# Kernel optimization log

Measured on AMD Instinct MI355X. Metric: run time of the kernel, lower is better.

## Reference

```python
import jax, jax.numpy as jnp
import numpy as np

N, E, IN_DIM, OUT_DIM, T = 100000, 1600000, 128, 64, 8
V_THRESHOLD = 1.0
EPS = 1e-7

# ---- Lorentz manifold (curvature -1), time coordinate first ----

def _linner(a, b):
    # Lorentzian inner product <a,b>_L = -a0*b0 + sum_i ai*bi
    return -a[..., 0] * b[..., 0] + jnp.sum(a[..., 1:] * b[..., 1:], axis=-1)

def _proju(z, u):
    # project ambient vector u to tangent space at z (<z,z>_L = -1)
    return u + _linner(z, u)[..., None] * z

def _expmap(z, u):
    un = jnp.sqrt(jnp.maximum(_linner(u, u), EPS))[..., None]
    return jnp.cosh(un) * z + jnp.sinh(un) * u / un

def _dist0(z):
    # geodesic distance to origin o=(1,0,...,0): arccosh(-<o,z>_L) = arccosh(z0)
    return jnp.arccosh(jnp.maximum(z[..., 0], 1.0 + EPS))

# ---- GCNConv (torch_geometric semantics: self-loops + symmetric norm) ----

def _gcn(x, edge_index, W, b):
    src, dst = edge_index[0], edge_index[1]
    loops = jnp.arange(N, dtype=src.dtype)
    src = jnp.concatenate([src, loops])
    dst = jnp.concatenate([dst, loops])
    deg = jax.ops.segment_sum(jnp.ones_like(dst, dtype=x.dtype), dst, num_segments=N)
    dinv = jax.lax.rsqrt(jnp.maximum(deg, 1.0))  # deg >= 1 due to self-loops
    norm = dinv[src] * dinv[dst]                 # [E+N]
    h = x @ W                                    # [N, OUT_DIM]
    out = jax.ops.segment_sum(norm[:, None] * h[src], dst, num_segments=N)
    return out + b


def setup_inputs() -> dict:
    key = jax.random.key(0)
    k1, k2, k3 = jax.random.split(key, 3)
    x = jax.random.normal(k1, (N, IN_DIM), dtype=jnp.float32)
    edge_index = jax.random.randint(k2, (2, E), 0, N, dtype=jnp.int32)
    W = jax.random.normal(k3, (IN_DIM, OUT_DIM), dtype=jnp.float32) / np.sqrt(IN_DIM)
    b = jnp.zeros((OUT_DIM,), dtype=jnp.float32)
    return {"x": x, "edge_index": edge_index, "W": W, "b": b}


def reference(x, edge_index, W, b):
    h = _gcn(x, edge_index, W, b)                       # [N, D]
    origin = jnp.zeros_like(h).at[..., 0].set(1.0)      # manifold origin
    x_seq = jnp.broadcast_to(h, (T,) + h.shape)         # [T, N, D]

    def step(z, x_t):
        u = _proju(z, x_t)                              # input current in T_z M
        z_new = _expmap(z, u)                           # charge along geodesic
        v = _dist0(z_new)                               # membrane potential [N]
        spike = v >= V_THRESHOLD
        z_out = jnp.where(spike[..., None], origin, z_new)  # hard reset
        return z_out, (spike.astype(h.dtype), z_out)

    _, (o_seq, z_seq) = jax.lax.scan(step, origin, x_seq)
    return o_seq, z_seq  # [T, N], [T, N, D]
```

## Files before the change

### kernel.cpp

```cpp
#include <hip/hip_runtime.h>
#include <math.h>

#define IN_DIM_C 128
#define OUT_DIM_C 64
#define T_STEPS 8
#define KC_MAX 512
#define PTILE 2048
#define GKC 32

__device__ __forceinline__ float4 f4zero() { return make_float4(0.f, 0.f, 0.f, 0.f); }

__global__ __launch_bounds__(64) void k_scanK(const int* __restrict__ chist,
                                              int* __restrict__ gcursor,
                                              int* __restrict__ offsets,
                                              int kc, int n, int E) {
    int lane = threadIdx.x;
    int carry = 0;
    for (int c = 0; c * 64 < kc; ++c) {
        int idx = c * 64 + lane;
        int v = (idx < kc) ? chist[idx] : 0;
        int x = v;
        #pragma unroll
        for (int off = 1; off < 64; off <<= 1) {
            int t = __shfl_up(x, off, 64);
            if (lane >= off) x += t;
        }
        if (idx < kc) gcursor[idx] = carry + x - v;
        carry += __shfl(x, 63, 64);
    }
    if (lane == 0) offsets[n] = E;
}

__global__ __launch_bounds__(256) void k_gemm_hist(const float* __restrict__ x,
                                                   const float* __restrict__ W,
                                                   float* __restrict__ h,
                                                   const int* __restrict__ dst,
                                                   int* __restrict__ chist,
                                                   int n, int E, int gemm_blocks) {
    __shared__ __align__(16) float smem[GKC * 132 + GKC * OUT_DIM_C];

    if ((int)blockIdx.x < gemm_blocks) {
        float* xs = smem;
        float* Ws = smem + GKC * 132;
        const int tid = threadIdx.x;
        const int cg = tid & 7;
        const int ng = tid >> 3;
        const int node_base = blockIdx.x * 128;

        float acc[4][8];
        #pragma unroll
        for (int i = 0; i < 4; ++i)
            #pragma unroll
            for (int j = 0; j < 8; ++j) acc[i][j] = 0.f;

        #pragma unroll 1
        for (int c = 0; c < IN_DIM_C / GKC; ++c) {
            __syncthreads();
            #pragma unroll
            for (int i = 0; i < 4; ++i) {
                int idx = tid + i * 256;
                int nd = idx >> 3, k4 = idx & 7;
                int node = node_base + nd;
                float4 v = f4zero();
                if (node < n) v = *(const float4*)&x[(long)node * IN_DIM_C + c * GKC + k4 * 4];
                xs[(k4 * 4 + 0) * 132 + nd] = v.x;
                xs[(k4 * 4 + 1) * 132 + nd] = v.y;
                xs[(k4 * 4 + 2) * 132 + nd] = v.z;
                xs[(k4 * 4 + 3) * 132 + nd] = v.w;
            }
            #pragma unroll
            for (int i = 0; i < 2; ++i) {
                int idx = tid + i * 256;
                ((float4*)Ws)[idx] = ((const float4*)&W[c * GKC * OUT_DIM_C])[idx];
            }
            __syncthreads();

            #pragma unroll
            for (int k = 0; k < GKC; ++k) {
                float4 a = *(const float4*)&xs[k * 132 + ng * 4];
                const float* wr = &Ws[k * OUT_DIM_C + cg * 8];
                float4 b0 = *(const float4*)&wr[0];
                float4 b1 = *(const float4*)&wr[4];
                #pragma unroll
                for (int i = 0; i < 4; ++i) {
                    float av = (i == 0) ? a.x : (i == 1) ? a.y : (i == 2) ? a.z : a.w;
                    acc[i][0] = fmaf(av, b0.x, acc[i][0]);
                    acc[i][1] = fmaf(av, b0.y, acc[i][1]);
                    acc[i][2] = fmaf(av, b0.z, acc[i][2]);
                    acc[i][3] = fmaf(av, b0.w, acc[i][3]);
                    acc[i][4] = fmaf(av, b1.x, acc[i][4]);
                    acc[i][5] = fmaf(av, b1.y, acc[i][5]);
                    acc[i][6] = fmaf(av, b1.z, acc[i][6]);
                    acc[i][7] = fmaf(av, b1.w, acc[i][7]);
                }
            }
        }

        #pragma unroll
        for (int i = 0; i < 4; ++i) {
            int node = node_base + ng * 4 + i;
            if (node < n) {
                *(float4*)&h[(long)node * OUT_DIM_C + cg * 8] =
                    make_float4(acc[i][0], acc[i][1], acc[i][2], acc[i][3]);
                *(float4*)&h[(long)node * OUT_DIM_C + cg * 8 + 4] =
                    make_float4(acc[i][4], acc[i][5], acc[i][6], acc[i][7]);
            }
        }
    } else {
        int* hh = (int*)smem;
        const int tid = threadIdx.x;
        int hb = blockIdx.x - gemm_blocks;
        for (int i = tid; i < KC_MAX; i += 256) hh[i] = 0;
        __syncthreads();
        long base = (long)hb * 4096;
        #pragma unroll
        for (int j = 0; j < 16; ++j) {
            long e = base + j * 256 + tid;
            if (e < E) atomicAdd(&hh[dst[e] >> 8], 1);
        }
        __syncthreads();
        for (int i = tid; i < KC_MAX; i += 256)
            if (hh[i]) atomicAdd(&chist[i], hh[i]);
    }
}

__global__ __launch_bounds__(256) void k_part(const int* __restrict__ src,
                                              const int* __restrict__ dst,
                                              int* __restrict__ gcursor,
                                              int* __restrict__ part, int E, int kc) {
    __shared__ int hist[KC_MAX];
    __shared__ int offs[KC_MAX];
    __shared__ int cur[KC_MAX];
    __shared__ int gbase[KC_MAX];
    const int tid = threadIdx.x;
    long base = (long)blockIdx.x * PTILE;

    for (int i = tid; i < KC_MAX; i += 256) hist[i] = 0;
    __syncthreads();
    #pragma unroll
    for (int j = 0; j < PTILE / 256; ++j) {
        long e = base + j * 256 + tid;
        if (e < E) atomicAdd(&hist[dst[e] >> 8], 1);
    }
    __syncthreads();
    if (tid < 64) {
        int carry = 0;
        for (int c = 0; c * 64 < kc; ++c) {
            int idx = c * 64 + tid;
            int v = (idx < kc) ? hist[idx] : 0;
            int x = v;
            #pragma unroll
            for (int off = 1; off < 64; off <<= 1) {
                int t = __shfl_up(x, off, 64);
                if (tid >= off) x += t;
            }
            if (idx < kc) { offs[idx] = carry + x - v; cur[idx] = carry + x - v; }
            carry += __shfl(x, 63, 64);
        }
    }
    __syncthreads();
    for (int b = tid; b < kc; b += 256)
        gbase[b] = hist[b] ? atomicAdd(&gcursor[b], hist[b]) : 0;
    __syncthreads();
    #pragma unroll
    for (int j = 0; j < PTILE / 256; ++j) {
        long e = base + j * 256 + tid;
        if (e < E) {
            int d = dst[e];
            int b = d >> 8;
            int r = atomicAdd(&cur[b], 1);
            part[gbase[b] + r - offs[b]] = (src[e] << 8) | (d & 255);
        }
    }
}

__global__ __launch_bounds__(256) void k_sort(const int* __restrict__ part,
                                              const int* __restrict__ gcursor,
                                              int* __restrict__ part2,
                                              int* __restrict__ offsets,
                                              float* __restrict__ dinv, int n) {
    __shared__ int cnt[256];
    __shared__ int cur[256];
    __shared__ int wsum[4], woff[4];
    const int tid = threadIdx.x;
    const int bkt = blockIdx.x;
    int start = bkt ? gcursor[bkt - 1] : 0;
    int end = gcursor[bkt];

    cnt[tid] = 0;
    __syncthreads();
    for (int i = start + tid; i < end; i += 256)
        atomicAdd(&cnt[part[i] & 255], 1);
    __syncthreads();

    int v = cnt[tid];
    int lane = tid & 63, wv = tid >> 6;
    int x = v;
    #pragma unroll
    for (int off = 1; off < 64; off <<= 1) {
        int t = __shfl_up(x, off, 64);
        if (lane >= off) x += t;
    }
    if (lane == 63) wsum[wv] = x;
    __syncthreads();
    if (tid == 0) { int c = 0; for (int w = 0; w < 4; ++w) { woff[w] = c; c += wsum[w]; } }
    __syncthreads();
    int myloc = woff[wv] + x - v;
    cur[tid] = myloc;
    int node = (bkt << 8) + tid;
    if (node < n) {
        offsets[node] = start + myloc;
        dinv[node] = rsqrtf((float)(v + 1));
    }
    __syncthreads();

    for (int i = start + tid; i < end; i += 256) {
        int p = part[i];
        int r = atomicAdd(&cur[p & 255], 1);
        part2[start + r] = ((unsigned)p) >> 8;
    }
}

__global__ __launch_bounds__(256) void k_pullspike(const int* __restrict__ offsets,
                                                   const int* __restrict__ part2,
                                                   const float* __restrict__ dinv,
                                                   const float* __restrict__ h,
                                                   const float* __restrict__ b,
                                                   float* __restrict__ o_seq,
                                                   float* __restrict__ z_seq, int n) {
    int gid = blockIdx.x * 256 + threadIdx.x;
    int node = gid >> 4;
    int sub = threadIdx.x & 15;
    if (node >= n) return;
    const float s0 = (sub == 0) ? -1.0f : 1.0f;
    int lane0 = (threadIdx.x & 63) & ~15;

    int o0 = offsets[node], o1 = offsets[node + 1];
    float dd = dinv[node];
    float4 hv = *(const float4*)&h[(long)node * OUT_DIM_C + sub * 4];
    float4 bv = *(const float4*)&b[sub * 4];
    float dd2 = dd * dd;
    float4 g = make_float4(fmaf(dd2, hv.x, bv.x), fmaf(dd2, hv.y, bv.y),
                           fmaf(dd2, hv.z, bv.z), fmaf(dd2, hv.w, bv.w));
    int i = o0;
    for (; i + 8 <= o1; i += 8) {
        int sa0 = part2[i],     sa1 = part2[i + 1], sa2 = part2[i + 2], sa3 = part2[i + 3];
        int sa4 = part2[i + 4], sa5 = part2[i + 5], sa6 = part2[i + 6], sa7 = part2[i + 7];
        float w0 = dinv[sa0] * dd, w1 = dinv[sa1] * dd, w2 = dinv[sa2] * dd, w3 = dinv[sa3] * dd;
        float w4 = dinv[sa4] * dd, w5 = dinv[sa5] * dd, w6 = dinv[sa6] * dd, w7 = dinv[sa7] * dd;
        float4 h0 = *(const float4*)&h[(long)sa0 * OUT_DIM_C + sub * 4];
        float4 h1 = *(const float4*)&h[(long)sa1 * OUT_DIM_C + sub * 4];
        float4 h2 = *(const float4*)&h[(long)sa2 * OUT_DIM_C + sub * 4];
        float4 h3 = *(const float4*)&h[(long)sa3 * OUT_DIM_C + sub * 4];
        float4 h4 = *(const float4*)&h[(long)sa4 * OUT_DIM_C + sub * 4];
        float4 h5 = *(const float4*)&h[(long)sa5 * OUT_DIM_C + sub * 4];
        float4 h6 = *(const float4*)&h[(long)sa6 * OUT_DIM_C + sub * 4];
        float4 h7 = *(const float4*)&h[(long)sa7 * OUT_DIM_C + sub * 4];
        g.x = fmaf(w0, h0.x, g.x); g.y = fmaf(w0, h0.y, g.y);
        g.z = fmaf(w0, h0.z, g.z); g.w = fmaf(w0, h0.w, g.w);
        g.x = fmaf(w1, h1.x, g.x); g.y = fmaf(w1, h1.y, g.y);
        g.z = fmaf(w1, h1.z, g.z); g.w = fmaf(w1, h1.w, g.w);
        g.x = fmaf(w2, h2.x, g.x); g.y = fmaf(w2, h2.y, g.y);
        g.z = fmaf(w2, h2.z, g.z); g.w = fmaf(w2, h2.w, g.w);
        g.x = fmaf(w3, h3.x, g.x); g.y = fmaf(w3, h3.y, g.y);
        g.z = fmaf(w3, h3.z, g.z); g.w = fmaf(w3, h3.w, g.w);
        g.x = fmaf(w4, h4.x, g.x); g.y = fmaf(w4, h4.y, g.y);
        g.z = fmaf(w4, h4.z, g.z); g.w = fmaf(w4, h4.w, g.w);
        g.x = fmaf(w5, h5.x, g.x); g.y = fmaf(w5, h5.y, g.y);
        g.z = fmaf(w5, h5.z, g.z); g.w = fmaf(w5, h5.w, g.w);
        g.x = fmaf(w6, h6.x, g.x); g.y = fmaf(w6, h6.y, g.y);
        g.z = fmaf(w6, h6.z, g.z); g.w = fmaf(w6, h6.w, g.w);
        g.x = fmaf(w7, h7.x, g.x); g.y = fmaf(w7, h7.y, g.y);
        g.z = fmaf(w7, h7.z, g.z); g.w = fmaf(w7, h7.w, g.w);
    }
    for (; i + 4 <= o1; i += 4) {
        int sa0 = part2[i], sa1 = part2[i + 1], sa2 = part2[i + 2], sa3 = part2[i + 3];
        float w0 = dinv[sa0] * dd, w1 = dinv[sa1] * dd;
        float w2 = dinv[sa2] * dd, w3 = dinv[sa3] * dd;
        float4 h0 = *(const float4*)&h[(long)sa0 * OUT_DIM_C + sub * 4];
        float4 h1 = *(const float4*)&h[(long)sa1 * OUT_DIM_C + sub * 4];
        float4 h2 = *(const float4*)&h[(long)sa2 * OUT_DIM_C + sub * 4];
        float4 h3 = *(const float4*)&h[(long)sa3 * OUT_DIM_C + sub * 4];
        g.x = fmaf(w0, h0.x, g.x); g.y = fmaf(w0, h0.y, g.y);
        g.z = fmaf(w0, h0.z, g.z); g.w = fmaf(w0, h0.w, g.w);
        g.x = fmaf(w1, h1.x, g.x); g.y = fmaf(w1, h1.y, g.y);
        g.z = fmaf(w1, h1.z, g.z); g.w = fmaf(w1, h1.w, g.w);
        g.x = fmaf(w2, h2.x, g.x); g.y = fmaf(w2, h2.y, g.y);
        g.z = fmaf(w2, h2.z, g.z); g.w = fmaf(w2, h2.w, g.w);
        g.x = fmaf(w3, h3.x, g.x); g.y = fmaf(w3, h3.y, g.y);
        g.z = fmaf(w3, h3.z, g.z); g.w = fmaf(w3, h3.w, g.w);
    }
    for (; i < o1; ++i) {
        int s = part2[i];
        float w = dinv[s] * dd;
        float4 h0 = *(const float4*)&h[(long)s * OUT_DIM_C + sub * 4];
        g.x = fmaf(w, h0.x, g.x); g.y = fmaf(w, h0.y, g.y);
        g.z = fmaf(w, h0.z, g.z); g.w = fmaf(w, h0.w, g.w);
    }

    float4 origin = f4zero();
    if (sub == 0) origin.x = 1.0f;

    auto step = [&](float4 z, float4& zn, bool& sp) {
        float p = s0 * z.x * g.x + z.y * g.y + z.z * g.z + z.w * g.w;
        p += __shfl_xor(p, 1, 64);
        p += __shfl_xor(p, 2, 64);
        p += __shfl_xor(p, 4, 64);
        p += __shfl_xor(p, 8, 64);
        float4 u = make_float4(fmaf(p, z.x, g.x), fmaf(p, z.y, g.y),
                               fmaf(p, z.z, g.z), fmaf(p, z.w, g.w));
        float q = s0 * u.x * u.x + u.y * u.y + u.z * u.z + u.w * u.w;
        q += __shfl_xor(q, 1, 64);
        q += __shfl_xor(q, 2, 64);
        q += __shfl_xor(q, 4, 64);
        q += __shfl_xor(q, 8, 64);
        float un = sqrtf(fmaxf(q, 1e-7f));
        float c = coshf(un);
        float sh = sinhf(un) / un;
        zn = make_float4(fmaf(c, z.x, sh * u.x), fmaf(c, z.y, sh * u.y),
                         fmaf(c, z.z, sh * u.z), fmaf(c, z.w, sh * u.w));
        float z0 = __shfl(zn.x, lane0, 64);
        float v = acoshf(fmaxf(z0, 1.0f + 1e-7f));
        sp = (v >= 1.0f);
    };

    float4 z1; bool sp0;
    step(origin, z1, sp0);
    float4 r0 = sp0 ? origin : z1;

    float4 z = origin;
    bool at0 = true;
    for (int t = 0; t < T_STEPS; ++t) {
        float4 zn; bool sp;
        if (at0) { sp = sp0; zn = r0; }
        else {
            step(z, zn, sp);
            if (sp) zn = origin;
        }
        *(float4*)&z_seq[(long)t * n * OUT_DIM_C + (long)node * OUT_DIM_C + sub * 4] = zn;
        if (sub == 0) o_seq[(long)t * n + node] = sp ? 1.0f : 0.0f;
        z = zn;
        at0 = sp;
    }
}

__global__ __launch_bounds__(256) void k_hist(const int* __restrict__ dst,
                                              int* __restrict__ chist, int E) {
    __shared__ int hh[KC_MAX];
    const int tid = threadIdx.x;
    for (int i = tid; i < KC_MAX; i += 256) hh[i] = 0;
    __syncthreads();
    long base = (long)blockIdx.x * 4096;
    #pragma unroll
    for (int j = 0; j < 16; ++j) {
        long e = base + j * 256 + tid;
        if (e < E) atomicAdd(&hh[dst[e] >> 8], 1);
    }
    __syncthreads();
    for (int i = tid; i < KC_MAX; i += 256)
        if (hh[i]) atomicAdd(&chist[i], hh[i]);
}

__global__ __launch_bounds__(256) void k_gemm(const float* __restrict__ x,
                                              const float* __restrict__ W,
                                              float* __restrict__ h, int n) {
    __shared__ __align__(16) float xs[GKC * 132];
    __shared__ __align__(16) float Ws[GKC * OUT_DIM_C];

    const int tid = threadIdx.x;
    const int cg = tid & 7;
    const int ng = tid >> 3;
    const int node_base = blockIdx.x * 128;

    float acc[4][8];
    #pragma unroll
    for (int i = 0; i < 4; ++i)
        #pragma unroll
        for (int j = 0; j < 8; ++j) acc[i][j] = 0.f;

    #pragma unroll 1
    for (int c = 0; c < IN_DIM_C / GKC; ++c) {
        __syncthreads();
        #pragma unroll
        for (int i = 0; i < 4; ++i) {
            int idx = tid + i * 256;
            int nd = idx >> 3, k4 = idx & 7;
            int node = node_base + nd;
            float4 v = f4zero();
            if (node < n) v = *(const float4*)&x[(long)node * IN_DIM_C + c * GKC + k4 * 4];
            xs[(k4 * 4 + 0) * 132 + nd] = v.x;
            xs[(k4 * 4 + 1) * 132 + nd] = v.y;
            xs[(k4 * 4 + 2) * 132 + nd] = v.z;
            xs[(k4 * 4 + 3) * 132 + nd] = v.w;
        }
        #pragma unroll
        for (int i = 0; i < 2; ++i) {
            int idx = tid + i * 256;
            ((float4*)Ws)[idx] = ((const float4*)&W[c * GKC * OUT_DIM_C])[idx];
        }
        __syncthreads();

        #pragma unroll
        for (int k = 0; k < GKC; ++k) {
            float4 a = *(const float4*)&xs[k * 132 + ng * 4];
            const float* wr = &Ws[k * OUT_DIM_C + cg * 8];
            float4 b0 = *(const float4*)&wr[0];
            float4 b1 = *(const float4*)&wr[4];
            #pragma unroll
            for (int i = 0; i < 4; ++i) {
                float av = (i == 0) ? a.x : (i == 1) ? a.y : (i == 2) ? a.z : a.w;
                acc[i][0] = fmaf(av, b0.x, acc[i][0]);
                acc[i][1] = fmaf(av, b0.y, acc[i][1]);
                acc[i][2] = fmaf(av, b0.z, acc[i][2]);
                acc[i][3] = fmaf(av, b0.w, acc[i][3]);
                acc[i][4] = fmaf(av, b1.x, acc[i][4]);
                acc[i][5] = fmaf(av, b1.y, acc[i][5]);
                acc[i][6] = fmaf(av, b1.z, acc[i][6]);
                acc[i][7] = fmaf(av, b1.w, acc[i][7]);
            }
        }
    }

    #pragma unroll
    for (int i = 0; i < 4; ++i) {
        int node = node_base + ng * 4 + i;
        if (node < n) {
            *(float4*)&h[(long)node * OUT_DIM_C + cg * 8] =
                make_float4(acc[i][0], acc[i][1], acc[i][2], acc[i][3]);
            *(float4*)&h[(long)node * OUT_DIM_C + cg * 8 + 4] =
                make_float4(acc[i][4], acc[i][5], acc[i][6], acc[i][7]);
        }
    }
}

__global__ __launch_bounds__(256) void k_pull(const int* __restrict__ offsets,
                                              const int* __restrict__ part2,
                                              const float* __restrict__ dinv,
                                              const float* __restrict__ h,
                                              const float* __restrict__ b,
                                              float* __restrict__ agg, int n) {
    int node = (blockIdx.x * 256 + threadIdx.x) >> 6;
    int lane = threadIdx.x & 63;
    if (node >= n) return;
    int o0 = offsets[node], o1 = offsets[node + 1];
    float dd = dinv[node];
    float acc = fmaf(dd * dd, h[(long)node * OUT_DIM_C + lane], b[lane]);
    int i = o0;
    for (; i + 4 <= o1; i += 4) {
        int s0 = part2[i], s1 = part2[i + 1], s2 = part2[i + 2], s3 = part2[i + 3];
        float n0 = dinv[s0] * dd, n1 = dinv[s1] * dd, n2 = dinv[s2] * dd, n3 = dinv[s3] * dd;
        acc = fmaf(n0, h[(long)s0 * OUT_DIM_C + lane], acc);
        acc = fmaf(n1, h[(long)s1 * OUT_DIM_C + lane], acc);
        acc = fmaf(n2, h[(long)s2 * OUT_DIM_C + lane], acc);
        acc = fmaf(n3, h[(long)s3 * OUT_DIM_C + lane], acc);
    }
    for (; i < o1; ++i) {
        int s = part2[i];
        acc = fmaf(dinv[s] * dd, h[(long)s * OUT_DIM_C + lane], acc);
    }
    agg[(long)node * OUT_DIM_C + lane] = acc;
}

__global__ __launch_bounds__(256) void k_spike(const float* agg,
                                               float* o_seq, float* z_seq, int n) {
    int gid = blockIdx.x * 256 + threadIdx.x;
    int node = gid >> 4;
    int sub = threadIdx.x & 15;
    if (node >= n) return;
    const float s0 = (sub == 0) ? -1.0f : 1.0f;
    int lane0 = (threadIdx.x & 63) & ~15;

    float4 g = *(const float4*)&agg[(long)node * OUT_DIM_C + sub * 4];
    float4 origin = f4zero();
    if (sub == 0) origin.x = 1.0f;

    auto step = [&](float4 z, float4& zn, bool& sp) {
        float p = s0 * z.x * g.x + z.y * g.y + z.z * g.z + z.w * g.w;
        p += __shfl_xor(p, 1, 64);
        p += __shfl_xor(p, 2, 64);
        p += __shfl_xor(p, 4, 64);
        p += __shfl_xor(p, 8, 64);
        float4 u = make_float4(fmaf(p, z.x, g.x), fmaf(p, z.y, g.y),
                               fmaf(p, z.z, g.z), fmaf(p, z.w, g.w));
        float q = s0 * u.x * u.x + u.y * u.y + u.z * u.z + u.w * u.w;
        q += __shfl_xor(q, 1, 64);
        q += __shfl_xor(q, 2, 64);
        q += __shfl_xor(q, 4, 64);
        q += __shfl_xor(q, 8, 64);
        float un = sqrtf(fmaxf(q, 1e-7f));
        float c = coshf(un);
        float sh = sinhf(un) / un;
        zn = make_float4(fmaf(c, z.x, sh * u.x), fmaf(c, z.y, sh * u.y),
                         fmaf(c, z.z, sh * u.z), fmaf(c, z.w, sh * u.w));
        float z0 = __shfl(zn.x, lane0, 64);
        float v = acoshf(fmaxf(z0, 1.0f + 1e-7f));
        sp = (v >= 1.0f);
    };

    float4 z1; bool sp0;
    step(origin, z1, sp0);
    float4 r0 = sp0 ? origin : z1;

    float4 z = origin;
    bool at0 = true;
    for (int t = 0; t < T_STEPS; ++t) {
        float4 zn; bool sp;
        if (at0) { sp = sp0; zn = r0; }
        else {
            step(z, zn, sp);
            if (sp) zn = origin;
        }
        *(float4*)&z_seq[(long)t * n * OUT_DIM_C + (long)node * OUT_DIM_C + sub * 4] = zn;
        if (sub == 0) o_seq[(long)t * n + node] = sp ? 1.0f : 0.0f;
        z = zn;
        at0 = sp;
    }
}

static inline size_t align256(size_t x) { return (x + 255) & ~(size_t)255; }

extern "C" void kernel_launch(void* const* d_in, const int* in_sizes, int n_in,
                              void* d_out, int out_size, void* d_ws, size_t ws_size,
                              hipStream_t stream) {
    const float* x  = (const float*)d_in[0];
    const int*   ei = (const int*)d_in[1];
    const float* W  = (const float*)d_in[2];
    const float* b  = (const float*)d_in[3];
    const int N = in_sizes[0] / IN_DIM_C;
    const int E = in_sizes[1] / 2;
    const int KC = (N + 255) >> 8;

    float* out   = (float*)d_out;
    float* o_seq = out;
    float* z_seq = out + (long)T_STEPS * N;

    const int* srcp = ei;
    const int* dstp = ei + E;

    size_t off_h    = 0;
    size_t off_p2   = align256(off_h + (size_t)N * OUT_DIM_C * 4);
    size_t off_offs = align256(off_p2 + (size_t)E * 4);
    size_t off_dinv = align256(off_offs + (size_t)(N + 1) * 4);
    size_t need     = align256(off_dinv + (size_t)N * 4);

    const int GB = (N + 127) / 128;
    const int HB = (E + 4095) / 4096;

    if (d_ws != nullptr && ws_size >= need) {
        float* h       = (float*)((char*)d_ws + off_h);
        int*   part2   = (int*)((char*)d_ws + off_p2);
        int*   offsets = (int*)((char*)d_ws + off_offs);
        float* dinv    = (float*)((char*)d_ws + off_dinv);
        int*   part    = (int*)(z_seq + 0L * N * OUT_DIM_C);
        int*   chist   = (int*)(z_seq + 1L * N * OUT_DIM_C);
        int*   gcursor = chist + KC_MAX;

        hipMemsetAsync(chist, 0, (size_t)KC_MAX * sizeof(int), stream);
        k_gemm_hist<<<GB + HB, 256, 0, stream>>>(x, W, h, dstp, chist, N, E, GB);
        k_scanK<<<1, 64, 0, stream>>>(chist, gcursor, offsets, KC, N, E);

        k_part<<<(E + PTILE - 1) / PTILE, 256, 0, stream>>>(srcp, dstp, gcursor, part, E, KC);
        k_sort<<<KC, 256, 0, stream>>>(part, gcursor, part2, offsets, dinv, N);

        k_pullspike<<<(N + 15) / 16, 256, 0, stream>>>(offsets, part2, dinv, h, b,
                                                       o_seq, z_seq, N);
    } else {
        float* agg     = z_seq;
        float* h       = z_seq + 1L * N * OUT_DIM_C;
        int*   part    = (int*)(z_seq + 2L * N * OUT_DIM_C);
        int*   part2   = (int*)(z_seq + 3L * N * OUT_DIM_C);
        int*   chist   = (int*)(z_seq + 4L * N * OUT_DIM_C);
        int*   gcursor = chist + KC_MAX;
        int*   offsets = gcursor + KC_MAX;
        float* dinv    = (float*)(offsets + N + 1);

        hipMemsetAsync(chist, 0, (size_t)KC_MAX * sizeof(int), stream);
        k_hist<<<HB, 256, 0, stream>>>(dstp, chist, E);
        k_scanK<<<1, 64, 0, stream>>>(chist, gcursor, offsets, KC, N, E);

        k_gemm<<<GB, 256, 0, stream>>>(x, W, h, N);

        k_part<<<(E + PTILE - 1) / PTILE, 256, 0, stream>>>(srcp, dstp, gcursor, part, E, KC);
        k_sort<<<KC, 256, 0, stream>>>(part, gcursor, part2, offsets, dinv, N);
        k_pull<<<(N * 64 + 255) / 256, 256, 0, stream>>>(offsets, part2, dinv, h, b, agg, N);

        k_spike<<<(N + 15) / 16, 256, 0, stream>>>(agg, o_seq, z_seq, N);
    }
}
```

Baseline: 396.9 us.

## Drop the separate bucket-scan kernel and enlarge GEMM tiles to 256 nodes per block

New measurement: 409.2 us. +3.1%, slower.

```diff
diff --git a/kernel.cpp b/kernel.cpp
--- a/kernel.cpp
+++ b/kernel.cpp
@@ -7,29 +7,9 @@
 #define KC_MAX 512
 #define PTILE 2048
 #define GKC 32
+#define XSTR 260
 
 __device__ __forceinline__ float4 f4zero() { return make_float4(0.f, 0.f, 0.f, 0.f); }
-
-__global__ __launch_bounds__(64) void k_scanK(const int* __restrict__ chist,
-                                              int* __restrict__ gcursor,
-                                              int* __restrict__ offsets,
-                                              int kc, int n, int E) {
-    int lane = threadIdx.x;
-    int carry = 0;
-    for (int c = 0; c * 64 < kc; ++c) {
-        int idx = c * 64 + lane;
-        int v = (idx < kc) ? chist[idx] : 0;
-        int x = v;
-        #pragma unroll
-        for (int off = 1; off < 64; off <<= 1) {
-            int t = __shfl_up(x, off, 64);
-            if (lane >= off) x += t;
-        }
-        if (idx < kc) gcursor[idx] = carry + x - v;
-        carry += __shfl(x, 63, 64);
-    }
-    if (lane == 0) offsets[n] = E;
-}
 
 __global__ __launch_bounds__(256) void k_gemm_hist(const float* __restrict__ x,
                                                    const float* __restrict__ W,
@@ -37,19 +17,19 @@
                                                    const int* __restrict__ dst,
                                                    int* __restrict__ chist,
                                                    int n, int E, int gemm_blocks) {
-    __shared__ __align__(16) float smem[GKC * 132 + GKC * OUT_DIM_C];
+    __shared__ __align__(16) float smem[GKC * XSTR + GKC * OUT_DIM_C];
 
     if ((int)blockIdx.x < gemm_blocks) {
         float* xs = smem;
-        float* Ws = smem + GKC * 132;
+        float* Ws = smem + GKC * XSTR;
         const int tid = threadIdx.x;
         const int cg = tid & 7;
         const int ng = tid >> 3;
-        const int node_base = blockIdx.x * 128;
-
-        float acc[4][8];
-        #pragma unroll
-        for (int i = 0; i < 4; ++i)
+        const int node_base = blockIdx.x * 256;
+
+        float acc[8][8];
+        #pragma unroll
+        for (int i = 0; i < 8; ++i)
             #pragma unroll
             for (int j = 0; j < 8; ++j) acc[i][j] = 0.f;
 
@@ -57,16 +37,16 @@
         for (int c = 0; c < IN_DIM_C / GKC; ++c) {
             __syncthreads();
             #pragma unroll
-            for (int i = 0; i < 4; ++i) {
+            for (int i = 0; i < 8; ++i) {
                 int idx = tid + i * 256;
                 int nd = idx >> 3, k4 = idx & 7;
                 int node = node_base + nd;
                 float4 v = f4zero();
                 if (node < n) v = *(const float4*)&x[(long)node * IN_DIM_C + c * GKC + k4 * 4];
-                xs[(k4 * 4 + 0) * 132 + nd] = v.x;
-                xs[(k4 * 4 + 1) * 132 + nd] = v.y;
-                xs[(k4 * 4 + 2) * 132 + nd] = v.z;
-                xs[(k4 * 4 + 3) * 132 + nd] = v.w;
+                xs[(k4 * 4 + 0) * XSTR + nd] = v.x;
+                xs[(k4 * 4 + 1) * XSTR + nd] = v.y;
+                xs[(k4 * 4 + 2) * XSTR + nd] = v.z;
+                xs[(k4 * 4 + 3) * XSTR + nd] = v.w;
             }
             #pragma unroll
             for (int i = 0; i < 2; ++i) {
@@ -75,15 +55,18 @@
             }
             __syncthreads();
 
-            #pragma unroll
+            #pragma unroll 4
             for (int k = 0; k < GKC; ++k) {
-                float4 a = *(const float4*)&xs[k * 132 + ng * 4];
+                float4 a0 = *(const float4*)&xs[k * XSTR + ng * 8];
+                float4 a1 = *(const float4*)&xs[k * XSTR + ng * 8 + 4];
                 const float* wr = &Ws[k * OUT_DIM_C + cg * 8];
                 float4 b0 = *(const float4*)&wr[0];
                 float4 b1 = *(const float4*)&wr[4];
                 #pragma unroll
-                for (int i = 0; i < 4; ++i) {
-                    float av = (i == 0) ? a.x : (i == 1) ? a.y : (i == 2) ? a.z : a.w;
+                for (int i = 0; i < 8; ++i) {
+                    float av = (i == 0) ? a0.x : (i == 1) ? a0.y : (i == 2) ? a0.z
+                             : (i == 3) ? a0.w : (i == 4) ? a1.x : (i == 5) ? a1.y
+                             : (i == 6) ? a1.z : a1.w;
                     acc[i][0] = fmaf(av, b0.x, acc[i][0]);
                     acc[i][1] = fmaf(av, b0.y, acc[i][1]);
                     acc[i][2] = fmaf(av, b0.z, acc[i][2]);
@@ -97,8 +80,8 @@
         }
 
         #pragma unroll
-        for (int i = 0; i < 4; ++i) {
-            int node = node_base + ng * 4 + i;
+        for (int i = 0; i < 8; ++i) {
+            int node = node_base + ng * 8 + i;
             if (node < n) {
                 *(float4*)&h[(long)node * OUT_DIM_C + cg * 8] =
                     make_float4(acc[i][0], acc[i][1], acc[i][2], acc[i][3]);
@@ -126,12 +109,14 @@
 
 __global__ __launch_bounds__(256) void k_part(const int* __restrict__ src,
                                               const int* __restrict__ dst,
+                                              const int* __restrict__ chist,
                                               int* __restrict__ gcursor,
                                               int* __restrict__ part, int E, int kc) {
     __shared__ int hist[KC_MAX];
     __shared__ int offs[KC_MAX];
     __shared__ int cur[KC_MAX];
     __shared__ int gbase[KC_MAX];
+    __shared__ int pref[KC_MAX];
     const int tid = threadIdx.x;
     long base = (long)blockIdx.x * PTILE;
 
@@ -144,23 +129,30 @@
     }
     __syncthreads();
     if (tid < 64) {
-        int carry = 0;
+        int carry = 0, carryG = 0;
         for (int c = 0; c * 64 < kc; ++c) {
             int idx = c * 64 + tid;
-            int v = (idx < kc) ? hist[idx] : 0;
-            int x = v;
+            int v  = (idx < kc) ? hist[idx] : 0;
+            int vg = (idx < kc) ? chist[idx] : 0;
+            int x = v, xg = vg;
             #pragma unroll
             for (int off = 1; off < 64; off <<= 1) {
-                int t = __shfl_up(x, off, 64);
-                if (tid >= off) x += t;
-            }
-            if (idx < kc) { offs[idx] = carry + x - v; cur[idx] = carry + x - v; }
-            carry += __shfl(x, 63, 64);
+                int t  = __shfl_up(x, off, 64);
+                int tg = __shfl_up(xg, off, 64);
+                if (tid >= off) { x += t; xg += tg; }
+            }
+            if (idx < kc) {
+                offs[idx] = carry + x - v;
+                cur[idx]  = carry + x - v;
+                pref[idx] = carryG + xg - vg;
+            }
+            carry  += __shfl(x, 63, 64);
+            carryG += __shfl(xg, 63, 64);
         }
     }
     __syncthreads();
     for (int b = tid; b < kc; b += 256)
-        gbase[b] = hist[b] ? atomicAdd(&gcursor[b], hist[b]) : 0;
+        gbase[b] = hist[b] ? pref[b] + atomicAdd(&gcursor[b], hist[b]) : 0;
     __syncthreads();
     #pragma unroll
     for (int j = 0; j < PTILE / 256; ++j) {
@@ -175,20 +167,31 @@
 }
 
 __global__ __launch_bounds__(256) void k_sort(const int* __restrict__ part,
-                                              const int* __restrict__ gcursor,
+                                              const int* __restrict__ chist,
                                               int* __restrict__ part2,
                                               int* __restrict__ offsets,
-                                              float* __restrict__ dinv, int n) {
+                                              float* __restrict__ dinv,
+                                              int n, int E, int kc) {
     __shared__ int cnt[256];
     __shared__ int cur[256];
     __shared__ int wsum[4], woff[4];
+    __shared__ int sred[4];
+    __shared__ int sstart;
     const int tid = threadIdx.x;
     const int bkt = blockIdx.x;
-    int start = bkt ? gcursor[bkt - 1] : 0;
-    int end = gcursor[bkt];
-
+
+    int s = 0;
+    for (int i = tid; i < bkt; i += 256) s += chist[i];
+    #pragma unroll
+    for (int m = 1; m < 64; m <<= 1) s += __shfl_xor(s, m, 64);
+    if ((tid & 63) == 0) sred[tid >> 6] = s;
     cnt[tid] = 0;
     __syncthreads();
+    if (tid == 0) sstart = sred[0] + sred[1] + sred[2] + sred[3];
+    __syncthreads();
+    const int start = sstart;
+    const int end = start + chist[bkt];
+
     for (int i = start + tid; i < end; i += 256)
         atomicAdd(&cnt[part[i] & 255], 1);
     __syncthreads();
@@ -212,6 +215,7 @@
         offsets[node] = start + myloc;
         dinv[node] = rsqrtf((float)(v + 1));
     }
+    if (bkt == kc - 1 && tid == 0) offsets[n] = E;
     __syncthreads();
 
     for (int i = start + tid; i < end; i += 256) {
@@ -291,9 +295,9 @@
         g.z = fmaf(w3, h3.z, g.z); g.w = fmaf(w3, h3.w, g.w);
     }
     for (; i < o1; ++i) {
-        int s = part2[i];
-        float w = dinv[s] * dd;
-        float4 h0 = *(const float4*)&h[(long)s * OUT_DIM_C + sub * 4];
+        int sidx = part2[i];
+        float w = dinv[sidx] * dd;
+        float4 h0 = *(const float4*)&h[(long)sidx * OUT_DIM_C + sub * 4];
         g.x = fmaf(w, h0.x, g.x); g.y = fmaf(w, h0.y, g.y);
         g.z = fmaf(w, h0.z, g.z); g.w = fmaf(w, h0.w, g.w);
     }
@@ -543,7 +547,7 @@
     size_t off_dinv = align256(off_offs + (size_t)(N + 1) * 4);
     size_t need     = align256(off_dinv + (size_t)N * 4);
 
-    const int GB = (N + 127) / 128;
+    const int GB = (N + 255) / 256;
     const int HB = (E + 4095) / 4096;
 
     if (d_ws != nullptr && ws_size >= need) {
@@ -555,13 +559,11 @@
         int*   chist   = (int*)(z_seq + 1L * N * OUT_DIM_C);
         int*   gcursor = chist + KC_MAX;
 
-        hipMemsetAsync(chist, 0, (size_t)KC_MAX * sizeof(int), stream);
+        hipMemsetAsync(chist, 0, (size_t)2 * KC_MAX * sizeof(int), stream);
         k_gemm_hist<<<GB + HB, 256, 0, stream>>>(x, W, h, dstp, chist, N, E, GB);
-        k_scanK<<<1, 64, 0, stream>>>(chist, gcursor, offsets, KC, N, E);
-
-        k_part<<<(E + PTILE - 1) / PTILE, 256, 0, stream>>>(srcp, dstp, gcursor, part, E, KC);
-        k_sort<<<KC, 256, 0, stream>>>(part, gcursor, part2, offsets, dinv, N);
-
+        k_part<<<(E + PTILE - 1) / PTILE, 256, 0, stream>>>(srcp, dstp, chist, gcursor,
+                                                            part, E, KC);
+        k_sort<<<KC, 256, 0, stream>>>(part, chist, part2, offsets, dinv, N, E, KC);
         k_pullspike<<<(N + 15) / 16, 256, 0, stream>>>(offsets, part2, dinv, h, b,
                                                        o_seq, z_seq, N);
     } else {
@@ -574,16 +576,13 @@
         int*   offsets = gcursor + KC_MAX;
         float* dinv    = (float*)(offsets + N + 1);
 
-        hipMemsetAsync(chist, 0, (size_t)KC_MAX * sizeof(int), stream);
+        hipMemsetAsync(chist, 0, (size_t)2 * KC_MAX * sizeof(int), stream);
         k_hist<<<HB, 256, 0, stream>>>(dstp, chist, E);
-        k_scanK<<<1, 64, 0, stream>>>(chist, gcursor, offsets, KC, N, E);
-
-        k_gemm<<<GB, 256, 0, stream>>>(x, W, h, N);
-
-        k_part<<<(E + PTILE - 1) / PTILE, 256, 0, stream>>>(srcp, dstp, gcursor, part, E, KC);
-        k_sort<<<KC, 256, 0, stream>>>(part, gcursor, part2, offsets, dinv, N);
+        k_gemm<<<(N + 127) / 128, 256, 0, stream>>>(x, W, h, N);
+        k_part<<<(E + PTILE - 1) / PTILE, 256, 0, stream>>>(srcp, dstp, chist, gcursor,
+                                                            part, E, KC);
+        k_sort<<<KC, 256, 0, stream>>>(part, chist, part2, offsets, dinv, N, E, KC);
         k_pull<<<(N * 64 + 255) / 256, 256, 0, stream>>>(offsets, part2, dinv, h, b, agg, N);
-
         k_spike<<<(N + 15) / 16, 256, 0, stream>>>(agg, o_seq, z_seq, N);
     }
 }
```
